# Kernel tuning notes

Hardware: AMD Instinct MI355X
Metric: run time of the kernel (lower is better)

## Reference

```python
import jax, jax.numpy as jnp
import numpy as np

N_NODES = 100000


def setup_inputs() -> dict:
    key = jax.random.key(0)
    k1, k2, k3 = jax.random.split(key, 3)
    feat = jax.random.normal(k1, (N_NODES, 64), dtype=jnp.float32)
    src = jax.random.randint(k2, (1250000,), 0, N_NODES, dtype=jnp.int64)
    dst = jax.random.randint(k3, (1250000,), 0, N_NODES, dtype=jnp.int64)
    return {"feat": feat, "src": src, "dst": dst}


def reference(feat, src, dst):
    # GraphConv(norm='both', activation=None): degree-normalized neighbor sum
    # with implicit self-connection (rst = feat_dst + sum_neighbors), where
    # degrees are clamp(min=1) + 1 to account for the self edge.
    n = feat.shape[0]
    ones = jnp.ones(src.shape[0], dtype=feat.dtype)
    out_deg = jax.ops.segment_sum(ones, src, num_segments=n)
    in_deg = jax.ops.segment_sum(ones, dst, num_segments=n)
    norm_l = jax.lax.rsqrt(jnp.maximum(out_deg, 1.0) + 1.0)  # [N]
    norm_r = jax.lax.rsqrt(jnp.maximum(in_deg, 1.0) + 1.0)   # [N]
    feat_src = feat * norm_l[:, None]                         # left-normalize
    msgs = feat_src[src]                                      # gather [E, D]
    h_neigh = jax.ops.segment_sum(msgs, dst, num_segments=n)  # scatter-sum [N, D]
    rst = (feat + h_neigh) * norm_r[:, None]                  # right-normalize
    return rst
```

## Files before the change

### kernel.cpp

```cpp
#include <hip/hip_runtime.h>


#define GC_D 64
#define GC_CAP 64
#define PBITS 8
#define PSIZE 256
#define SCAP 4096
#define EPB 8192


__global__ void zero_int_kernel(int* __restrict__ p, int n) {
    int i = blockIdx.x * blockDim.x + threadIdx.x;
    if (i < n) p[i] = 0;
}

__global__ __launch_bounds__(512) void partition_kernel(
        const int* __restrict__ src,
        const int* __restrict__ dst,
        int* __restrict__ curA,
        int* __restrict__ curB,
        int* __restrict__ streamA,
        unsigned char* __restrict__ streamB,
        int e, int nPart) {
    __shared__ int histA[512], histB[512], baseA[512], baseB[512];
    __shared__ int lcurA[512], lcurB[512];
    int t = threadIdx.x;
    for (int i = t; i < nPart; i += 512) {
        histA[i] = 0; histB[i] = 0; lcurA[i] = 0; lcurB[i] = 0;
    }
    __syncthreads();
    int lo = blockIdx.x * EPB;
    int hi = min(lo + EPB, e);
    for (int i = lo + t; i < hi; i += 512) {
        int s = src[i], d = dst[i];
        atomicAdd(&histA[d >> PBITS], 1);
        atomicAdd(&histB[s >> PBITS], 1);
    }
    __syncthreads();
    for (int i = t; i < nPart; i += 512) {
        int hA = histA[i];
        baseA[i] = hA ? atomicAdd(&curA[i], hA) : 0;
        int hB = histB[i];
        baseB[i] = hB ? atomicAdd(&curB[i], hB) : 0;
    }
    __syncthreads();
    for (int i = lo + t; i < hi; i += 512) {
        int s = src[i], d = dst[i];
        int pA = d >> PBITS;
        int posA = baseA[pA] + atomicAdd(&lcurA[pA], 1);
        if (posA < SCAP) streamA[pA * SCAP + posA] = s | ((d & 255) << 17);
        int pB = s >> PBITS;
        int posB = baseB[pB] + atomicAdd(&lcurB[pB], 1);
        if (posB < SCAP) streamB[pB * SCAP + posB] = (unsigned char)(s & 255);
    }
}

__global__ __launch_bounds__(256) void build_kernel(
        const int* __restrict__ curA,
        const int* __restrict__ curB,
        const int* __restrict__ streamA,
        const unsigned char* __restrict__ streamB,
        int* __restrict__ cnt,
        int* __restrict__ outdeg,
        int* __restrict__ bucket,
        int n) {
    __shared__ int lcnt[PSIZE], lodeg[PSIZE], lcur[PSIZE];
    __shared__ int lbucket[PSIZE * GC_CAP];
    int p = blockIdx.x;
    int t = threadIdx.x;
    lcnt[t] = 0; lodeg[t] = 0; lcur[t] = 0;
    __syncthreads();
    int cA = min(curA[p], SCAP);
    int cB = min(curB[p], SCAP);
    const int* sA = streamA + (size_t)p * SCAP;
    const unsigned char* sB = streamB + (size_t)p * SCAP;
    for (int i = t; i < cA; i += 256) {
        int entry = sA[i];
        int bin = (entry >> 17) & 255;
        atomicAdd(&lcnt[bin], 1);
        int pos = atomicAdd(&lcur[bin], 1);
        if (pos < GC_CAP) lbucket[bin * GC_CAP + pos] = entry & 0x1FFFF;
    }
    for (int i = t; i < cB; i += 256) atomicAdd(&lodeg[sB[i]], 1);
    __syncthreads();
    int g = p * PSIZE + t;
    if (g < n) { cnt[g] = lcnt[t]; outdeg[g] = lodeg[t]; }
    int4* dstw = (int4*)(bucket + (size_t)p * PSIZE * GC_CAP);
    const int4* srcw = (const int4*)lbucket;
#pragma unroll
    for (int i = 0; i < (PSIZE * GC_CAP / 4) / 256; ++i)
        dstw[i * 256 + t] = srcw[i * 256 + t];
}

__global__ void convert_kernel(const float* __restrict__ feat,
                               const int* __restrict__ outdeg,
                               unsigned short* __restrict__ featb,
                               int n) {
    int i = blockIdx.x * blockDim.x + threadIdx.x;
    int total = (n + 1) * GC_D;
    if (i >= total) return;
    int row = i >> 6;
    if (row >= n) { featb[i] = 0; return; }
    float nl = rsqrtf(fmaxf((float)outdeg[row], 1.0f) + 1.0f);
    unsigned b = __float_as_uint(feat[i] * nl);
    b = (b + 0x7FFFu + ((b >> 16) & 1u)) >> 16;
    featb[i] = (unsigned short)b;
}

__global__ __launch_bounds__(256) void gather_bf16_kernel(
        const float* __restrict__ feat,
        const unsigned short* __restrict__ featb,
        const int* __restrict__ bucket,
        const int* __restrict__ cnt,
        float* __restrict__ out,
        int n) {
    int wid = (blockIdx.x * blockDim.x + threadIdx.x) >> 6;
    int lane = threadIdx.x & 63;
    if (wid >= n) return;
    int deg = cnt[wid];
    int s_raw = bucket[wid * GC_CAP + lane];
    int m = min(deg, GC_CAP);
    int s_l = (lane < m) ? s_raw : n;
    int half = lane >> 5;
    int c = lane & 31;
    float acc0 = 0.0f, acc1 = 0.0f;
    int m16 = (m + 15) & ~15;
    for (int j = 0; j < m16; j += 16) {
#pragma unroll
        for (int k = 0; k < 8; ++k) {
            int s = __shfl(s_l, j + 2 * k + half);
            unsigned u = *(const unsigned*)(featb + (size_t)s * GC_D + 2 * c);
            acc0 += __uint_as_float(u << 16);
            acc1 += __uint_as_float(u & 0xFFFF0000u);
        }
    }
    acc0 += __shfl_xor(acc0, 32);
    acc1 += __shfl_xor(acc1, 32);
    if (half == 0) {
        float nr = rsqrtf(fmaxf((float)deg, 1.0f) + 1.0f);
        const float2 self = *(const float2*)(feat + (size_t)wid * GC_D + 2 * c);
        float2 r;
        r.x = (self.x + acc0) * nr;
        r.y = (self.y + acc1) * nr;
        *(float2*)(out + (size_t)wid * GC_D + 2 * c) = r;
    }
}


__global__ void bucket_hist_kernel(const int* __restrict__ src,
                                   const int* __restrict__ dst,
                                   int* __restrict__ cnt,
                                   int* __restrict__ outdeg,
                                   int* __restrict__ bucket,
                                   int e) {
    int i = blockIdx.x * blockDim.x + threadIdx.x;
    if (i < e) {
        int s = src[i];
        int d = dst[i];
        atomicAdd(&outdeg[s], 1);
        int pos = atomicAdd(&cnt[d], 1);
        if (pos < GC_CAP) bucket[d * GC_CAP + pos] = s;
    }
}


__global__ void hist_kernel(const int* __restrict__ src,
                            const int* __restrict__ dst,
                            int* __restrict__ outdeg,
                            int* __restrict__ indeg,
                            int e) {
    int i = blockIdx.x * blockDim.x + threadIdx.x;
    if (i < e) {
        atomicAdd(&outdeg[src[i]], 1);
        atomicAdd(&indeg[dst[i]], 1);
    }
}

__global__ void block_reduce_kernel(const int* __restrict__ indeg,
                                    int* __restrict__ partials,
                                    int n) {
    __shared__ int sdata[256];
    int t = threadIdx.x;
    int i = blockIdx.x * 256 + t;
    sdata[t] = (i < n) ? indeg[i] : 0;
    __syncthreads();
    for (int s = 128; s > 0; s >>= 1) {
        if (t < s) sdata[t] += sdata[t + s];
        __syncthreads();
    }
    if (t == 0) partials[blockIdx.x] = sdata[0];
}

__global__ void scan_partials_kernel(const int* __restrict__ partials,
                                     int* __restrict__ scanned,
                                     int P) {
    __shared__ int sdata[512];
    int t = threadIdx.x;
    int own = (t < P) ? partials[t] : 0;
    sdata[t] = own;
    __syncthreads();
    for (int off = 1; off < 512; off <<= 1) {
        int v = (t >= off) ? sdata[t - off] : 0;
        __syncthreads();
        sdata[t] += v;
        __syncthreads();
    }
    if (t < P) scanned[t] = sdata[t] - own;
}

__global__ void scan_final_kernel(const int* __restrict__ indeg,
                                  const int* __restrict__ outdeg,
                                  const int* __restrict__ scanned,
                                  int* __restrict__ offsets,
                                  int* __restrict__ cursors,
                                  float* __restrict__ norm_l,
                                  float* __restrict__ norm_r,
                                  int n) {
    __shared__ int sdata[256];
    int t = threadIdx.x;
    int i = blockIdx.x * 256 + t;
    int c = (i < n) ? indeg[i] : 0;
    sdata[t] = c;
    __syncthreads();
    for (int off = 1; off < 256; off <<= 1) {
        int v = (t >= off) ? sdata[t - off] : 0;
        __syncthreads();
        sdata[t] += v;
        __syncthreads();
    }
    if (i < n) {
        int excl = sdata[t] - c;
        int pos = scanned[blockIdx.x] + excl;
        offsets[i] = pos;
        cursors[i] = pos;
        norm_r[i] = rsqrtf(fmaxf((float)c, 1.0f) + 1.0f);
        norm_l[i] = rsqrtf(fmaxf((float)outdeg[i], 1.0f) + 1.0f);
    }
}

__global__ void bucket_kernel(const int* __restrict__ src,
                              const int* __restrict__ dst,
                              int* __restrict__ cursors,
                              int* __restrict__ perm_src,
                              int e) {
    int i = blockIdx.x * blockDim.x + threadIdx.x;
    if (i < e) {
        int d = dst[i];
        int pos = atomicAdd(&cursors[d], 1);
        perm_src[pos] = src[i];
    }
}

__global__ __launch_bounds__(256) void gather_csr_kernel(
        const float* __restrict__ feat,
        const int* __restrict__ perm_src,
        const int* __restrict__ offsets,
        const int* __restrict__ indeg,
        const float* __restrict__ norm_l,
        const float* __restrict__ norm_r,
        float* __restrict__ out,
        int n) {
    int wid = (blockIdx.x * blockDim.x + threadIdx.x) >> 6;
    int lane = threadIdx.x & 63;
    if (wid >= n) return;
    int off = offsets[wid];
    int deg = indeg[wid];
    float acc = 0.0f;
    for (int base = 0; base < deg; base += 64) {
        int m = min(64, deg - base);
        int s_l = 0;
        float nl_l = 0.0f;
        if (lane < m) {
            s_l = perm_src[off + base + lane];
            nl_l = norm_l[s_l];
        }
        for (int j = 0; j < m; ++j) {
            int s = __shfl(s_l, j);
            float nl = __shfl(nl_l, j);
            acc += feat[s * GC_D + lane] * nl;
        }
    }
    int oi = wid * GC_D + lane;
    out[oi] = (feat[oi] + acc) * norm_r[wid];
}


extern "C" void kernel_launch(void* const* d_in, const int* in_sizes, int n_in,
                              void* d_out, int out_size, void* d_ws, size_t ws_size,
                              hipStream_t stream) {
    const float* feat = (const float*)d_in[0];
    const int*   src  = (const int*)d_in[1];
    const int*   dst  = (const int*)d_in[2];
    float* out = (float*)d_out;

    const int n = in_sizes[0] / GC_D;
    const int e = in_sizes[1];
    const int P = (n + 255) / 256;
    const int nPart = (n + PSIZE - 1) >> PBITS;

    size_t bucket_ints   = (size_t)nPart * PSIZE * GC_CAP;
    size_t streams_bytes = (size_t)nPart * SCAP * (sizeof(int) + 1);
    size_t featb_bytes   = (size_t)(n + 1) * GC_D * sizeof(unsigned short);
    size_t region_bytes  = streams_bytes > featb_bytes ? streams_bytes : featb_bytes;
    size_t need_part = ((size_t)2 * nPart + (size_t)2 * n + bucket_ints)
                       * sizeof(int) + region_bytes;
    size_t need_bf16 = ((size_t)2 * n + (size_t)n * GC_CAP) * sizeof(int) + featb_bytes;
    size_t need_csr = ((size_t)6 * n + 2 * P + e) * sizeof(int);

    if (ws_size >= need_part && nPart <= 512) {
        int* curA   = (int*)d_ws;
        int* curB   = curA + nPart;
        int* cnt    = curB + nPart;
        int* outdeg = cnt + n;
        int* bucket = outdeg + n;
        int* region = bucket + bucket_ints;
        int* streamA = region;
        unsigned char* streamB = (unsigned char*)(streamA + (size_t)nPart * SCAP);
        unsigned short* featb = (unsigned short*)region;

        zero_int_kernel<<<(2 * nPart + 255) / 256, 256, 0, stream>>>(curA, 2 * nPart);
        partition_kernel<<<(e + EPB - 1) / EPB, 512, 0, stream>>>(
            src, dst, curA, curB, streamA, streamB, e, nPart);
        build_kernel<<<nPart, 256, 0, stream>>>(curA, curB, streamA, streamB,
                                                cnt, outdeg, bucket, n);
        {
            int total = (n + 1) * GC_D;
            convert_kernel<<<(total + 255) / 256, 256, 0, stream>>>(feat, outdeg,
                                                                    featb, n);
        }
        {
            long long total = (long long)n * GC_D;
            gather_bf16_kernel<<<(int)((total + 255) / 256), 256, 0, stream>>>(
                feat, featb, bucket, cnt, out, n);
        }
    } else if (ws_size >= need_bf16) {
        int* cnt    = (int*)d_ws;
        int* outdeg = cnt + n;
        int* bucket = outdeg + n;
        unsigned short* featb = (unsigned short*)(bucket + (size_t)n * GC_CAP);

        zero_int_kernel<<<(2 * n + 255) / 256, 256, 0, stream>>>(cnt, 2 * n);
        bucket_hist_kernel<<<(e + 255) / 256, 256, 0, stream>>>(src, dst, cnt,
                                                                outdeg, bucket, e);
        {
            int total = (n + 1) * GC_D;
            convert_kernel<<<(total + 255) / 256, 256, 0, stream>>>(feat, outdeg,
                                                                    featb, n);
        }
        {
            long long total = (long long)n * GC_D;
            gather_bf16_kernel<<<(int)((total + 255) / 256), 256, 0, stream>>>(
                feat, featb, bucket, cnt, out, n);
        }
    } else if (ws_size >= need_csr && P <= 512) {
        int* indeg   = (int*)d_ws;
        int* outdeg  = indeg + n;
        int* offsets = outdeg + n;
        int* cursors = offsets + n;
        float* norm_l = (float*)(cursors + n);
        float* norm_r = norm_l + n;
        int* partials = (int*)(norm_r + n);
        int* scanned  = partials + P;
        int* perm_src = scanned + P;

        zero_int_kernel<<<(2 * n + 255) / 256, 256, 0, stream>>>(indeg, 2 * n);
        hist_kernel<<<(e + 255) / 256, 256, 0, stream>>>(src, dst, outdeg, indeg, e);
        block_reduce_kernel<<<P, 256, 0, stream>>>(indeg, partials, n);
        scan_partials_kernel<<<1, 512, 0, stream>>>(partials, scanned, P);
        scan_final_kernel<<<P, 256, 0, stream>>>(indeg, outdeg, scanned, offsets,
                                                 cursors, norm_l, norm_r, n);
        bucket_kernel<<<(e + 255) / 256, 256, 0, stream>>>(src, dst, cursors, perm_src, e);
        long long total = (long long)n * GC_D;
        gather_csr_kernel<<<(int)((total + 255) / 256), 256, 0, stream>>>(
            feat, perm_src, offsets, indeg, norm_l, norm_r, out, n);
    }
}
```

Baseline: 172.9 us.

## Replace global-atomic partitioning with per-block scanned streams and fuse bf16 conversion into build

The partition kernel now computes a per-block exclusive scan of partition counts in shared memory and writes each edge-block's entries contiguously, which removes the global atomic cursors, the zero-init kernel and the SCAP overflow cap. The build kernel reads per-block row offsets to walk each partition's slices across all edge blocks. It also performs the bf16 left-normalized conversion itself, using its shared out-degree counts, so the separate convert kernel and the outdeg round trip go away. In exchange the build kernel does a more scattered, serialized walk over many small slices, and the workspace now holds a rowScan table.

```diff
diff --git a/kernel.cpp b/kernel.cpp
--- a/kernel.cpp
+++ b/kernel.cpp
@@ -5,106 +5,124 @@
 #define GC_CAP 64
 #define PBITS 8
 #define PSIZE 256
-#define SCAP 4096
-#define EPB 8192
-
-
-__global__ void zero_int_kernel(int* __restrict__ p, int n) {
-    int i = blockIdx.x * blockDim.x + threadIdx.x;
-    if (i < n) p[i] = 0;
-}
+#define EPB 4096
+#define MAXPART 512
+
 
 __global__ __launch_bounds__(512) void partition_kernel(
         const int* __restrict__ src,
         const int* __restrict__ dst,
-        int* __restrict__ curA,
-        int* __restrict__ curB,
+        int* __restrict__ rowScanA,
+        int* __restrict__ rowScanB,
         int* __restrict__ streamA,
         unsigned char* __restrict__ streamB,
         int e, int nPart) {
-    __shared__ int histA[512], histB[512], baseA[512], baseB[512];
-    __shared__ int lcurA[512], lcurB[512];
-    int t = threadIdx.x;
-    for (int i = t; i < nPart; i += 512) {
-        histA[i] = 0; histB[i] = 0; lcurA[i] = 0; lcurB[i] = 0;
-    }
-    __syncthreads();
-    int lo = blockIdx.x * EPB;
+    __shared__ int curA[MAXPART], curB[MAXPART];
+    __shared__ int scanA[MAXPART], scanB[MAXPART];
+    int t = threadIdx.x, b = blockIdx.x;
+    for (int i = t; i < nPart; i += 512) { curA[i] = 0; curB[i] = 0; }
+    __syncthreads();
+    int lo = b * EPB;
     int hi = min(lo + EPB, e);
     for (int i = lo + t; i < hi; i += 512) {
         int s = src[i], d = dst[i];
-        atomicAdd(&histA[d >> PBITS], 1);
-        atomicAdd(&histB[s >> PBITS], 1);
-    }
-    __syncthreads();
-    for (int i = t; i < nPart; i += 512) {
-        int hA = histA[i];
-        baseA[i] = hA ? atomicAdd(&curA[i], hA) : 0;
-        int hB = histB[i];
-        baseB[i] = hB ? atomicAdd(&curB[i], hB) : 0;
-    }
-    __syncthreads();
+        atomicAdd(&curA[d >> PBITS], 1);
+        atomicAdd(&curB[s >> PBITS], 1);
+    }
+    __syncthreads();
+    int vA = (t < nPart) ? curA[t] : 0;
+    int vB = (t < nPart) ? curB[t] : 0;
+    scanA[t] = vA; scanB[t] = vB;
+    __syncthreads();
+    for (int off = 1; off < 512; off <<= 1) {
+        int aA = (t >= off) ? scanA[t - off] : 0;
+        int aB = (t >= off) ? scanB[t - off] : 0;
+        __syncthreads();
+        scanA[t] += aA; scanB[t] += aB;
+        __syncthreads();
+    }
+    long long rbase = (long long)b * (nPart + 1);
+    if (t < nPart) {
+        int exA = scanA[t] - vA, exB = scanB[t] - vB;
+        rowScanA[rbase + t] = exA;
+        rowScanB[rbase + t] = exB;
+        curA[t] = exA;
+        curB[t] = exB;
+        if (t == nPart - 1) {
+            rowScanA[rbase + nPart] = scanA[t];
+            rowScanB[rbase + nPart] = scanB[t];
+        }
+    }
+    __syncthreads();
+    int* sA = streamA + (long long)b * EPB;
+    unsigned char* sB = streamB + (long long)b * EPB;
     for (int i = lo + t; i < hi; i += 512) {
         int s = src[i], d = dst[i];
-        int pA = d >> PBITS;
-        int posA = baseA[pA] + atomicAdd(&lcurA[pA], 1);
-        if (posA < SCAP) streamA[pA * SCAP + posA] = s | ((d & 255) << 17);
-        int pB = s >> PBITS;
-        int posB = baseB[pB] + atomicAdd(&lcurB[pB], 1);
-        if (posB < SCAP) streamB[pB * SCAP + posB] = (unsigned char)(s & 255);
-    }
-}
-
-__global__ __launch_bounds__(256) void build_kernel(
-        const int* __restrict__ curA,
-        const int* __restrict__ curB,
+        int posA = atomicAdd(&curA[d >> PBITS], 1);
+        sA[posA] = s | ((d & 255) << 17);
+        int posB = atomicAdd(&curB[s >> PBITS], 1);
+        sB[posB] = (unsigned char)(s & 255);
+    }
+}
+
+__global__ __launch_bounds__(512) void build_kernel(
+        const int* __restrict__ rowScanA,
+        const int* __restrict__ rowScanB,
         const int* __restrict__ streamA,
         const unsigned char* __restrict__ streamB,
+        const float* __restrict__ feat,
         int* __restrict__ cnt,
-        int* __restrict__ outdeg,
+        unsigned short* __restrict__ featb,
         int* __restrict__ bucket,
-        int n) {
-    __shared__ int lcnt[PSIZE], lodeg[PSIZE], lcur[PSIZE];
+        int n, int nPart, int nBlk) {
+    __shared__ int lcur[PSIZE], lodeg[PSIZE];
     __shared__ int lbucket[PSIZE * GC_CAP];
-    int p = blockIdx.x;
-    int t = threadIdx.x;
-    lcnt[t] = 0; lodeg[t] = 0; lcur[t] = 0;
-    __syncthreads();
-    int cA = min(curA[p], SCAP);
-    int cB = min(curB[p], SCAP);
-    const int* sA = streamA + (size_t)p * SCAP;
-    const unsigned char* sB = streamB + (size_t)p * SCAP;
-    for (int i = t; i < cA; i += 256) {
-        int entry = sA[i];
-        int bin = (entry >> 17) & 255;
-        atomicAdd(&lcnt[bin], 1);
-        int pos = atomicAdd(&lcur[bin], 1);
-        if (pos < GC_CAP) lbucket[bin * GC_CAP + pos] = entry & 0x1FFFF;
-    }
-    for (int i = t; i < cB; i += 256) atomicAdd(&lodeg[sB[i]], 1);
-    __syncthreads();
-    int g = p * PSIZE + t;
-    if (g < n) { cnt[g] = lcnt[t]; outdeg[g] = lodeg[t]; }
+    int p = blockIdx.x, t = threadIdx.x;
+    if (t < PSIZE) { lcur[t] = 0; lodeg[t] = 0; }
+    __syncthreads();
+    int wave = t >> 6, lane = t & 63;
+    int nb = (nBlk + 7) >> 3;
+    int myb = wave + 8 * lane;
+    int offA = 0, endA = 0, offB = 0, endB = 0;
+    if (lane < nb && myb < nBlk) {
+        long long r = (long long)myb * (nPart + 1) + p;
+        offA = rowScanA[r]; endA = rowScanA[r + 1];
+        offB = rowScanB[r]; endB = rowScanB[r + 1];
+    }
+    for (int k = 0; k < nb; ++k) {
+        int b = wave + 8 * k;
+        if (b >= nBlk) break;
+        int oA = __shfl(offA, k), eA = __shfl(endA, k);
+        const int* sA = streamA + (long long)b * EPB;
+        for (int i = oA + lane; i < eA; i += 64) {
+            int entry = sA[i];
+            int bin = (entry >> 17) & 255;
+            int pos = atomicAdd(&lcur[bin], 1);
+            if (pos < GC_CAP) lbucket[bin * GC_CAP + pos] = entry & 0x1FFFF;
+        }
+        int oB = __shfl(offB, k), eB = __shfl(endB, k);
+        const unsigned char* sB = streamB + (long long)b * EPB;
+        for (int i = oB + lane; i < eB; i += 64)
+            atomicAdd(&lodeg[sB[i]], 1);
+    }
+    __syncthreads();
+    int g = p * PSIZE;
+    if (t < PSIZE && g + t < n) cnt[g + t] = lcur[t];
     int4* dstw = (int4*)(bucket + (size_t)p * PSIZE * GC_CAP);
     const int4* srcw = (const int4*)lbucket;
 #pragma unroll
-    for (int i = 0; i < (PSIZE * GC_CAP / 4) / 256; ++i)
-        dstw[i * 256 + t] = srcw[i * 256 + t];
-}
-
-__global__ void convert_kernel(const float* __restrict__ feat,
-                               const int* __restrict__ outdeg,
-                               unsigned short* __restrict__ featb,
-                               int n) {
-    int i = blockIdx.x * blockDim.x + threadIdx.x;
-    int total = (n + 1) * GC_D;
-    if (i >= total) return;
-    int row = i >> 6;
-    if (row >= n) { featb[i] = 0; return; }
-    float nl = rsqrtf(fmaxf((float)outdeg[row], 1.0f) + 1.0f);
-    unsigned b = __float_as_uint(feat[i] * nl);
-    b = (b + 0x7FFFu + ((b >> 16) & 1u)) >> 16;
-    featb[i] = (unsigned short)b;
+    for (int i = 0; i < (PSIZE * GC_CAP / 4) / 512; ++i)
+        dstw[i * 512 + t] = srcw[i * 512 + t];
+    for (int r = wave; r < PSIZE; r += 8) {
+        int node = g + r;
+        if (node >= n) break;
+        float nl = rsqrtf(fmaxf((float)lodeg[r], 1.0f) + 1.0f);
+        float v = feat[(size_t)node * GC_D + lane] * nl;
+        unsigned bb = __float_as_uint(v);
+        bb = (bb + 0x7FFFu + ((bb >> 16) & 1u)) >> 16;
+        featb[(size_t)node * GC_D + lane] = (unsigned short)bb;
+    }
+    if (p == 0 && t < GC_D) featb[(size_t)n * GC_D + t] = 0;
 }
 
 __global__ __launch_bounds__(256) void gather_bf16_kernel(
@@ -147,6 +165,11 @@
 }
 
 
+__global__ void zero_int_kernel(int* __restrict__ p, int n) {
+    int i = blockIdx.x * blockDim.x + threadIdx.x;
+    if (i < n) p[i] = 0;
+}
+
 __global__ void bucket_hist_kernel(const int* __restrict__ src,
                                    const int* __restrict__ dst,
                                    int* __restrict__ cnt,
@@ -161,6 +184,21 @@
         int pos = atomicAdd(&cnt[d], 1);
         if (pos < GC_CAP) bucket[d * GC_CAP + pos] = s;
     }
+}
+
+__global__ void convert_kernel(const float* __restrict__ feat,
+                               const int* __restrict__ outdeg,
+                               unsigned short* __restrict__ featb,
+                               int n) {
+    int i = blockIdx.x * blockDim.x + threadIdx.x;
+    int total = (n + 1) * GC_D;
+    if (i >= total) return;
+    int row = i >> 6;
+    if (row >= n) { featb[i] = 0; return; }
+    float nl = rsqrtf(fmaxf((float)outdeg[row], 1.0f) + 1.0f);
+    unsigned b = __float_as_uint(feat[i] * nl);
+    b = (b + 0x7FFFu + ((b >> 16) & 1u)) >> 16;
+    featb[i] = (unsigned short)b;
 }
 
 
@@ -297,42 +335,41 @@
     const int e = in_sizes[1];
     const int P = (n + 255) / 256;
     const int nPart = (n + PSIZE - 1) >> PBITS;
-
-    size_t bucket_ints   = (size_t)nPart * PSIZE * GC_CAP;
-    size_t streams_bytes = (size_t)nPart * SCAP * (sizeof(int) + 1);
-    size_t featb_bytes   = (size_t)(n + 1) * GC_D * sizeof(unsigned short);
-    size_t region_bytes  = streams_bytes > featb_bytes ? streams_bytes : featb_bytes;
-    size_t need_part = ((size_t)2 * nPart + (size_t)2 * n + bucket_ints)
-                       * sizeof(int) + region_bytes;
+    const int nBlk  = (e + EPB - 1) / EPB;
+
+    size_t rs_ints     = (size_t)nBlk * (nPart + 1);
+    size_t bucket_ints = (size_t)nPart * PSIZE * GC_CAP;
+    size_t featb_bytes = (size_t)(n + 1) * GC_D * sizeof(unsigned short);
+    size_t need_main = (2 * rs_ints + (size_t)nBlk * EPB + (size_t)n + bucket_ints)
+                       * sizeof(int) + featb_bytes + (size_t)nBlk * EPB + 64;
     size_t need_bf16 = ((size_t)2 * n + (size_t)n * GC_CAP) * sizeof(int) + featb_bytes;
     size_t need_csr = ((size_t)6 * n + 2 * P + e) * sizeof(int);
 
-    if (ws_size >= need_part && nPart <= 512) {
-        int* curA   = (int*)d_ws;
-        int* curB   = curA + nPart;
-        int* cnt    = curB + nPart;
-        int* outdeg = cnt + n;
-        int* bucket = outdeg + n;
-        int* region = bucket + bucket_ints;
-        int* streamA = region;
-        unsigned char* streamB = (unsigned char*)(streamA + (size_t)nPart * SCAP);
-        unsigned short* featb = (unsigned short*)region;
-
-        zero_int_kernel<<<(2 * nPart + 255) / 256, 256, 0, stream>>>(curA, 2 * nPart);
-        partition_kernel<<<(e + EPB - 1) / EPB, 512, 0, stream>>>(
-            src, dst, curA, curB, streamA, streamB, e, nPart);
-        build_kernel<<<nPart, 256, 0, stream>>>(curA, curB, streamA, streamB,
-                                                cnt, outdeg, bucket, n);
+    bool main_ok = (ws_size >= need_main) && nPart <= MAXPART && nBlk <= 512 &&
+                   n <= 131071;
+
+    if (main_ok) {
+        int* rowScanA = (int*)d_ws;
+        int* rowScanB = rowScanA + rs_ints;
+        int* streamA  = rowScanB + rs_ints;
+        int* cnt      = streamA + (size_t)nBlk * EPB;
+        int* bucket   = cnt + n;
         {
-            int total = (n + 1) * GC_D;
-            convert_kernel<<<(total + 255) / 256, 256, 0, stream>>>(feat, outdeg,
-                                                                    featb, n);
-        }
-        {
-            long long total = (long long)n * GC_D;
-            gather_bf16_kernel<<<(int)((total + 255) / 256), 256, 0, stream>>>(
-                feat, featb, bucket, cnt, out, n);
-        }
+            size_t off_ints = 2 * rs_ints + (size_t)nBlk * EPB + (size_t)n;
+            size_t pad = (4 - (off_ints & 3)) & 3;
+            bucket += pad;
+        }
+        unsigned short* featb = (unsigned short*)(bucket + bucket_ints);
+        unsigned char* streamB = (unsigned char*)(featb + (size_t)(n + 1) * GC_D);
+
+        partition_kernel<<<nBlk, 512, 0, stream>>>(src, dst, rowScanA, rowScanB,
+                                                   streamA, streamB, e, nPart);
+        build_kernel<<<nPart, 512, 0, stream>>>(rowScanA, rowScanB, streamA, streamB,
+                                                feat, cnt, featb, bucket,
+                                                n, nPart, nBlk);
+        long long total = (long long)n * GC_D;
+        gather_bf16_kernel<<<(int)((total + 255) / 256), 256, 0, stream>>>(
+            feat, featb, bucket, cnt, out, n);
     } else if (ws_size >= need_bf16) {
         int* cnt    = (int*)d_ws;
         int* outdeg = cnt + n;
@@ -342,16 +379,12 @@
         zero_int_kernel<<<(2 * n + 255) / 256, 256, 0, stream>>>(cnt, 2 * n);
         bucket_hist_kernel<<<(e + 255) / 256, 256, 0, stream>>>(src, dst, cnt,
                                                                 outdeg, bucket, e);
-        {
-            int total = (n + 1) * GC_D;
-            convert_kernel<<<(total + 255) / 256, 256, 0, stream>>>(feat, outdeg,
-                                                                    featb, n);
-        }
-        {
-            long long total = (long long)n * GC_D;
-            gather_bf16_kernel<<<(int)((total + 255) / 256), 256, 0, stream>>>(
-                feat, featb, bucket, cnt, out, n);
-        }
+        int totalc = (n + 1) * GC_D;
+        convert_kernel<<<(totalc + 255) / 256, 256, 0, stream>>>(feat, outdeg,
+                                                                 featb, n);
+        long long total = (long long)n * GC_D;
+        gather_bf16_kernel<<<(int)((total + 255) / 256), 256, 0, stream>>>(
+            feat, featb, bucket, cnt, out, n);
     } else if (ws_size >= need_csr && P <= 512) {
         int* indeg   = (int*)d_ws;
         int* outdeg  = indeg + n;
```

Result: slower. 185.6 us (+7.3%).
